# Performance work log

Hardware: AMD Instinct MI355X
Metric: run time of the kernel (lower is better)

The kernel has to match this reference:

```python
import jax, jax.numpy as jnp
import numpy as np

N = 100_000   # nodes
E = 600_000   # edges per layer (avg degree ~6, ogbn-arxiv-like)
IN, H, C = 128, 256, 40


def _sage_layer(x, src, dst, w_self, w_neigh, b):
    """DGL SAGEConv with mean aggregator: fc_self(x) + fc_neigh(mean_nbr) + b."""
    n = x.shape[0]
    msg = x[src]                                               # [E, d] gather
    agg = jax.ops.segment_sum(msg, dst, num_segments=n)        # [N, d]
    deg = jax.ops.segment_sum(jnp.ones((src.shape[0],), x.dtype), dst,
                              num_segments=n)                  # [N]
    h_neigh = agg / jnp.maximum(deg, 1.0)[:, None]             # mean; 0 if isolated
    return x @ w_self.T + h_neigh @ w_neigh.T + b


def setup_inputs() -> dict:
    key = jax.random.key(0)
    ks = jax.random.split(key, 11)
    s = 0.02
    return {
        "x": jax.random.normal(ks[0], (N, IN), jnp.float32),
        "src1": jax.random.randint(ks[1], (E,), 0, N, jnp.int32),
        "dst1": jax.random.randint(ks[2], (E,), 0, N, jnp.int32),
        "src2": jax.random.randint(ks[3], (E,), 0, N, jnp.int32),
        "dst2": jax.random.randint(ks[4], (E,), 0, N, jnp.int32),
        "w_self1": s * jax.random.normal(ks[5], (H, IN), jnp.float32),
        "w_neigh1": s * jax.random.normal(ks[6], (H, IN), jnp.float32),
        "b1": jnp.zeros((H,), jnp.float32),
        "w_self2": s * jax.random.normal(ks[7], (C, H), jnp.float32),
        "w_neigh2": s * jax.random.normal(ks[8], (C, H), jnp.float32),
        "b2": jnp.zeros((C,), jnp.float32),
    }


def reference(x, src1, dst1, src2, dst2, w_self1, w_neigh1, b1,
              w_self2, w_neigh2, b2):
    h = jax.nn.relu(_sage_layer(x, src1, dst1, w_self1, w_neigh1, b1))
    return _sage_layer(h, src2, dst2, w_self2, w_neigh2, b2)
```

## Files before the change

kernel.cpp:

```cpp
#include <hip/hip_runtime.h>
#include <hip/hip_bf16.h>
#include <cstdint>
#include <cstddef>


#define D_IN 128
#define D_H  256
#define D_C  40

#define NBLK     128
#define NBKT_MAX 392
#define BKT_CAP  2560

typedef __bf16 bf16_t;
typedef __attribute__((ext_vector_type(8))) __bf16 bf16x8;
typedef __attribute__((ext_vector_type(4))) float  f32x4;

static constexpr size_t NMAX = 100000;
static constexpr size_t EMAX = 600000;
static constexpr size_t NSC_MAX = (size_t)NBKT_MAX * NBLK;
static constexpr size_t alignup(size_t v) { return (v + 255) & ~size_t(255); }

static constexpr size_t HG1_OFF  = 0;
static constexpr size_t HG2_OFF  = alignup(HG1_OFF + NSC_MAX * 4);
static constexpr size_t BS1_OFF  = alignup(HG2_OFF + NSC_MAX * 4);
static constexpr size_t BS2_OFF  = alignup(BS1_OFF + 512 * 4);
static constexpr size_t RP1_OFF  = alignup(BS2_OFF + 512 * 4);
static constexpr size_t RP2_OFF  = alignup(RP1_OFF + (NMAX + 1) * 4);
static constexpr size_t BKT1_OFF = alignup(RP2_OFF + (NMAX + 1) * 4);
static constexpr size_t BKT2_OFF = alignup(BKT1_OFF + EMAX * 4);
static constexpr size_t XCAT_OFF = alignup(BKT2_OFF + EMAX * 4);
static constexpr size_t P_OFF    = alignup(XCAT_OFF + (NMAX + 64) * 256 * 2);
static constexpr size_t W1F_OFF  = alignup(P_OFF + NMAX * 40 * 4);
static constexpr size_t W2F_OFF  = alignup(W1F_OFF + 32 * 256 * 8 * 2);
static constexpr size_t WS_NEEDED = W2F_OFF + 32 * 80 * 8 * 2;

__global__ __launch_bounds__(256) void k_prep(
    const float* __restrict__ x, bf16_t* __restrict__ xcat,
    const float* __restrict__ ws1, const float* __restrict__ wn1,
    const float* __restrict__ ws2, const float* __restrict__ wn2,
    bf16_t* __restrict__ w1f, bf16_t* __restrict__ w2f,
    const int* __restrict__ dst1, const int* __restrict__ dst2,
    int* __restrict__ hg1, int* __restrict__ hg2,
    int N, int E, int chunk, int nbkt, int nconvx) {
  __shared__ int h[NBKT_MAX];
  int bid = blockIdx.x;

  if (bid < nconvx) {
    int t = bid * 256 + threadIdx.x;
    if (t < N * 16) {
      int row = t >> 4, j = t & 15;
      const float* sp = x + (size_t)row * 128 + j * 8;
      float4 v0 = ((const float4*)sp)[0];
      float4 v1 = ((const float4*)sp)[1];
      bf16x8 o;
      o[0] = (bf16_t)v0.x; o[1] = (bf16_t)v0.y; o[2] = (bf16_t)v0.z; o[3] = (bf16_t)v0.w;
      o[4] = (bf16_t)v1.x; o[5] = (bf16_t)v1.y; o[6] = (bf16_t)v1.z; o[7] = (bf16_t)v1.w;
      *(bf16x8*)(xcat + (size_t)row * 256 + j * 8) = o;
    }
    return;
  }
  bid -= nconvx;

  if (bid < 32) {
    int t = bid * 256 + threadIdx.x;
    {
      int ks4g = t >> 8, col = t & 255;
      int k0 = (ks4g >> 2) * 32 + (ks4g & 3) * 8;
      bf16x8 o;
#pragma unroll
      for (int i = 0; i < 8; ++i) {
        int k = k0 + i;
        float v = (k < 128) ? ws1[col * 128 + k] : wn1[col * 128 + (k - 128)];
        o[i] = (bf16_t)v;
      }
      *(bf16x8*)(w1f + (size_t)t * 8) = o;
    }
    if (t < 32 * 80) {
      int ks4g = t / 80, col = t - ks4g * 80;
      int k0 = (ks4g >> 2) * 32 + (ks4g & 3) * 8;
      bf16x8 o;
#pragma unroll
      for (int i = 0; i < 8; ++i) {
        int k = k0 + i;
        float v = (col < 40) ? ws2[col * 256 + k] : wn2[(col - 40) * 256 + k];
        o[i] = (bf16_t)v;
      }
      *(bf16x8*)(w2f + (size_t)t * 8) = o;
    }
    return;
  }
  bid -= 32;
  {
    const int* dst = (bid >> 7) ? dst2 : dst1;
    int*       hg  = (bid >> 7) ? hg2 : hg1;
    int        cb  = bid & 127;
    for (int i = threadIdx.x; i < nbkt; i += 256) h[i] = 0;
    __syncthreads();
    int beg = cb * chunk, end = min(E, beg + chunk);
    for (int e = beg + threadIdx.x; e < end; e += 256)
      atomicAdd(&h[dst[e] >> 8], 1);
    __syncthreads();
    for (int b = threadIdx.x; b < nbkt; b += 256)
      hg[b * NBLK + cb] = h[b];
  }
}

__global__ void k_scan_block(int* __restrict__ a1, int* __restrict__ a2,
                             int* __restrict__ b1s, int* __restrict__ b2s, int n) {
  int* a    = blockIdx.y ? a2 : a1;
  int* bsum = blockIdx.y ? b2s : b1s;
  __shared__ int lds[256];
  int t = threadIdx.x, i = blockIdx.x * 256 + t;
  int v = (i < n) ? a[i] : 0;
  lds[t] = v;
  __syncthreads();
  for (int off = 1; off < 256; off <<= 1) {
    int add = (t >= off) ? lds[t - off] : 0;
    __syncthreads();
    lds[t] += add;
    __syncthreads();
  }
  if (i < n) a[i] = lds[t] - v;
  if (t == 255) bsum[blockIdx.x] = lds[255];
}

__global__ void k_scan_sums(int* __restrict__ b1s, int* __restrict__ b2s, int nb) {
  int* bsum = blockIdx.x ? b2s : b1s;
  __shared__ int lds[512];
  int t = threadIdx.x;
  int v = (t < nb) ? bsum[t] : 0;
  lds[t] = v;
  __syncthreads();
  for (int off = 1; off < 512; off <<= 1) {
    int add = (t >= off) ? lds[t - off] : 0;
    __syncthreads();
    lds[t] += add;
    __syncthreads();
  }
  if (t < nb) bsum[t] = lds[t] - v;
}

__global__ void k_scan_add(int* __restrict__ a1, int* __restrict__ a2,
                           const int* __restrict__ b1s, const int* __restrict__ b2s, int n) {
  int* a        = blockIdx.y ? a2 : a1;
  const int* bs = blockIdx.y ? b2s : b1s;
  int i = blockIdx.x * 256 + threadIdx.x;
  if (i < n) a[i] += bs[i >> 8];
}

__global__ void k_scat(const int* __restrict__ src1, const int* __restrict__ dst1,
                       const int* __restrict__ src2, const int* __restrict__ dst2,
                       const int* __restrict__ off1, const int* __restrict__ off2,
                       unsigned* __restrict__ bkt1, unsigned* __restrict__ bkt2,
                       int E, int chunk, int nbkt) {
  const int* src = blockIdx.y ? src2 : src1;
  const int* dst = blockIdx.y ? dst2 : dst1;
  const int* off = blockIdx.y ? off2 : off1;
  unsigned*  bkt = blockIdx.y ? bkt2 : bkt1;
  __shared__ int cur[NBKT_MAX];
  for (int i = threadIdx.x; i < nbkt; i += 256)
    cur[i] = off[i * NBLK + blockIdx.x];
  __syncthreads();
  int beg = blockIdx.x * chunk, end = min(E, beg + chunk);
  for (int e = beg + threadIdx.x; e < end; e += 256) {
    int d = dst[e];
    int slot = atomicAdd(&cur[d >> 8], 1);
    bkt[slot] = (unsigned)src[e] | ((unsigned)(d & 255) << 24);
  }
}

__global__ __launch_bounds__(256) void k_bcsr(
    const int* __restrict__ off1, const int* __restrict__ off2,
    const unsigned* bkt1, const unsigned* bkt2,
    int* csr1, int* csr2,
    int* __restrict__ rp1, int* __restrict__ rp2, int E, int N, int nbkt) {
  const int* off      = blockIdx.y ? off2 : off1;
  const unsigned* bkt = blockIdx.y ? bkt2 : bkt1;
  int* csr            = blockIdx.y ? csr2 : csr1;
  int* rowptr         = blockIdx.y ? rp2 : rp1;

  const int b = blockIdx.x, t = threadIdx.x;
  const int base = off[b * NBLK];
  const int endp = (b == nbkt - 1) ? E : off[(b + 1) * NBLK];
  const int cnt  = endp - base;

  __shared__ int hist[256];
  __shared__ int sc[256];
  __shared__ int cur[256];
  __shared__ int stage[BKT_CAP];

  hist[t] = 0;
  __syncthreads();
  for (int i = t; i < cnt; i += 256)
    atomicAdd(&hist[bkt[base + i] >> 24], 1);
  __syncthreads();

  int v = hist[t];
  sc[t] = v;
  __syncthreads();
  for (int off_ = 1; off_ < 256; off_ <<= 1) {
    int add = (t >= off_) ? sc[t - off_] : 0;
    __syncthreads();
    sc[t] += add;
    __syncthreads();
  }
  int excl = sc[t] - v;

  int node = b * 256 + t;
  if (node < N) rowptr[node] = base + excl;
  if (b == nbkt - 1 && t == 0) rowptr[N] = E;
  cur[t] = excl;
  __syncthreads();

  for (int i = t; i < cnt; i += 256) {
    unsigned u = bkt[base + i];
    int slot = atomicAdd(&cur[u >> 24], 1);
    if (slot < BKT_CAP) stage[slot] = (int)(u & 0xFFFFFFu);
  }
  __syncthreads();
  for (int i = t; i < cnt; i += 256)
    csr[base + i] = stage[i];
}

__global__ void k_agg1(bf16_t* __restrict__ xcat, const int* __restrict__ rowptr,
                       const int* __restrict__ csr, int N) {
  int t = blockIdx.x * 256 + threadIdx.x;
  int node = t >> 4, l = t & 15;
  if (node >= N) return;
  int beg = rowptr[node], end = rowptr[node + 1];
  float acc[8] = {0.f, 0.f, 0.f, 0.f, 0.f, 0.f, 0.f, 0.f};
  for (int e = beg; e < end; ++e) {
    int s = csr[e];
    bf16x8 v = *(const bf16x8*)(xcat + (size_t)s * 256 + l * 8);
#pragma unroll
    for (int i = 0; i < 8; ++i) acc[i] += (float)v[i];
  }
  float rd = (end > beg) ? 1.0f / (float)(end - beg) : 0.0f;
  bf16x8 o;
#pragma unroll
  for (int i = 0; i < 8; ++i) o[i] = (bf16_t)(acc[i] * rd);
  *(bf16x8*)(xcat + (size_t)node * 256 + 128 + l * 8) = o;
}

__global__ __launch_bounds__(256, 4) void k_fused(
    const bf16_t* __restrict__ xcat, const bf16_t* __restrict__ w1f,
    const float* __restrict__ b1, const bf16_t* __restrict__ w2f,
    const float* __restrict__ b2v, float* __restrict__ out,
    float* __restrict__ p, int N) {
  __shared__ __align__(16) char lds[32768];
  const int m0   = blockIdx.x * 64;
  const int wv   = threadIdx.x >> 6;
  const int lane = threadIdx.x & 63;
  const int lr   = lane & 15;
  const int lg   = lane >> 4;
  const int c0   = wv * 64;

  {
    const char* tbase = (const char*)(xcat + (size_t)m0 * 256);
#pragma unroll
    for (int i = 0; i < 8; ++i) {
      int L   = i * 4096 + (int)threadIdx.x * 16;
      int row = L >> 9;
      int c   = L & 511;
      int so  = (row << 9) | (c ^ ((row & 7) << 4));
      __builtin_amdgcn_global_load_lds(
          (const __attribute__((address_space(1))) void*)(tbase + so),
          (__attribute__((address_space(3))) void*)(lds + L), 16, 0, 0);
    }
  }
  __syncthreads();

  f32x4 acc[4][4] = {};
#pragma unroll
  for (int ks = 0; ks < 8; ++ks) {
    bf16x8 a[4];
#pragma unroll
    for (int m = 0; m < 4; ++m) {
      int lrow = m * 16 + lr;
      int c    = ks * 64 + lg * 16;
      a[m] = *(const bf16x8*)(lds + lrow * 512 + (c ^ ((lrow & 7) << 4)));
    }
    bf16x8 b[4];
#pragma unroll
    for (int bn = 0; bn < 4; ++bn) {
      int col = c0 + bn * 16 + lr;
      b[bn] = *(const bf16x8*)(w1f + ((size_t)(ks * 4 + lg) * 256 + col) * 8);
    }
#pragma unroll
    for (int m = 0; m < 4; ++m)
#pragma unroll
      for (int bn = 0; bn < 4; ++bn)
        acc[m][bn] = __builtin_amdgcn_mfma_f32_16x16x32_bf16(a[m], b[bn], acc[m][bn], 0, 0, 0);
  }
  __syncthreads();

#pragma unroll
  for (int bn = 0; bn < 4; ++bn) {
    int   col  = c0 + bn * 16 + lr;
    float bias = b1[col];
#pragma unroll
    for (int m = 0; m < 4; ++m) {
#pragma unroll
      for (int i = 0; i < 4; ++i) {
        int row = m * 16 + lg * 4 + i;
        float v = acc[m][bn][i] + bias;
        *(bf16_t*)(lds + row * 512 + ((col * 2) ^ ((row & 7) << 4))) =
            (bf16_t)fmaxf(v, 0.0f);
      }
    }
  }
  __syncthreads();

  f32x4 acc2[5] = {};
  const int arow = wv * 16 + lr;
#pragma unroll
  for (int ks = 0; ks < 8; ++ks) {
    int c = ks * 64 + lg * 16;
    bf16x8 a2 = *(const bf16x8*)(lds + arow * 512 + (c ^ ((arow & 7) << 4)));
#pragma unroll
    for (int bn = 0; bn < 5; ++bn) {
      int col = bn * 16 + lr;
      bf16x8 bb = *(const bf16x8*)(w2f + ((size_t)(ks * 4 + lg) * 80 + col) * 8);
      acc2[bn] = __builtin_amdgcn_mfma_f32_16x16x32_bf16(a2, bb, acc2[bn], 0, 0, 0);
    }
  }

#pragma unroll
  for (int bn = 0; bn < 5; ++bn) {
    int col = bn * 16 + lr;
#pragma unroll
    for (int i = 0; i < 4; ++i) {
      int r = m0 + wv * 16 + lg * 4 + i;
      if (r < N) {
        float v = acc2[bn][i];
        if (col < 40) out[(size_t)r * 40 + col] = v + b2v[col];
        else          p[(size_t)r * 40 + (col - 40)] = v;
      }
    }
  }
}

__global__ void k_agg2fin(const float* __restrict__ p, const int* __restrict__ rowptr,
                          const int* __restrict__ csr, float* __restrict__ out, int N) {
  int t = blockIdx.x * 256 + threadIdx.x;
  int node = t / 10, l = t - node * 10;
  if (node >= N) return;
  int beg = rowptr[node], end = rowptr[node + 1];
  float4 acc = {0.f, 0.f, 0.f, 0.f};
  for (int e = beg; e < end; ++e) {
    int s = csr[e];
    float4 v = *(const float4*)(p + (size_t)s * 40 + l * 4);
    acc.x += v.x; acc.y += v.y; acc.z += v.z; acc.w += v.w;
  }
  float rd = (end > beg) ? 1.0f / (float)(end - beg) : 0.0f;
  float* o = out + (size_t)node * 40 + l * 4;
  float4 cur = *(const float4*)o;
  cur.x += acc.x * rd;
  cur.y += acc.y * rd;
  cur.z += acc.z * rd;
  cur.w += acc.w * rd;
  *(float4*)o = cur;
}

extern "C" void kernel_launch(void* const* d_in, const int* in_sizes, int n_in,
                              void* d_out, int out_size, void* d_ws, size_t ws_size,
                              hipStream_t stream) {
  const float* x    = (const float*)d_in[0];
  const int*   src1 = (const int*)d_in[1];
  const int*   dst1 = (const int*)d_in[2];
  const int*   src2 = (const int*)d_in[3];
  const int*   dst2 = (const int*)d_in[4];
  const float* ws1  = (const float*)d_in[5];
  const float* wn1  = (const float*)d_in[6];
  const float* b1   = (const float*)d_in[7];
  const float* ws2  = (const float*)d_in[8];
  const float* wn2  = (const float*)d_in[9];
  const float* b2   = (const float*)d_in[10];
  float*       out  = (float*)d_out;

  const int N = in_sizes[0] / D_IN;
  const int E = in_sizes[1];
  if (ws_size < WS_NEEDED) return;

  char*     ws   = (char*)d_ws;
  int*      hg1  = (int*)(ws + HG1_OFF);
  int*      hg2  = (int*)(ws + HG2_OFF);
  int*      bs1  = (int*)(ws + BS1_OFF);
  int*      bs2  = (int*)(ws + BS2_OFF);
  int*      rp1  = (int*)(ws + RP1_OFF);
  int*      rp2  = (int*)(ws + RP2_OFF);
  unsigned* bkt1 = (unsigned*)(ws + BKT1_OFF);
  unsigned* bkt2 = (unsigned*)(ws + BKT2_OFF);
  int*      csr1 = (int*)(ws + BKT1_OFF);
  int*      csr2 = (int*)(ws + BKT2_OFF);
  bf16_t*   xcat = (bf16_t*)(ws + XCAT_OFF);
  float*    p    = (float*)(ws + P_OFF);
  bf16_t*   w1f  = (bf16_t*)(ws + W1F_OFF);
  bf16_t*   w2f  = (bf16_t*)(ws + W2F_OFF);

  const int nbkt  = (N + 255) >> 8;
  const int chunk = (E + NBLK - 1) / NBLK;
  const int nsc   = nbkt * NBLK;
  const int nscb  = (nsc + 255) / 256;
  const int nconvx = (N * 16 + 255) / 256;

  k_prep<<<nconvx + 32 + 2 * NBLK, 256, 0, stream>>>(
      x, xcat, ws1, wn1, ws2, wn2, w1f, w2f, dst1, dst2, hg1, hg2,
      N, E, chunk, nbkt, nconvx);

  k_scan_block<<<dim3(nscb, 2), 256, 0, stream>>>(hg1, hg2, bs1, bs2, nsc);
  k_scan_sums<<<2, 512, 0, stream>>>(bs1, bs2, nscb);
  k_scan_add<<<dim3(nscb, 2), 256, 0, stream>>>(hg1, hg2, bs1, bs2, nsc);
  k_scat<<<dim3(NBLK, 2), 256, 0, stream>>>(src1, dst1, src2, dst2, hg1, hg2,
                                            bkt1, bkt2, E, chunk, nbkt);
  k_bcsr<<<dim3(nbkt, 2), 256, 0, stream>>>(hg1, hg2, bkt1, bkt2, csr1, csr2,
                                            rp1, rp2, E, N, nbkt);

  k_agg1<<<(N * 16 + 255) / 256, 256, 0, stream>>>(xcat, rp1, csr1, N);
  k_fused<<<(N + 63) / 64, 256, 0, stream>>>(xcat, w1f, b1, w2f, b2, out, p, N);
  k_agg2fin<<<(N * 10 + 255) / 256, 256, 0, stream>>>(p, rp2, csr2, out, N);
}
```

Before: 151.9 us.

## Make fused GEMM kernel persistent with double-buffered LDS tile prefetch

Turns the fused two-layer GEMM kernel into a persistent kernel with a grid capped at 512 blocks. Each block loops over 64-row tiles and prefetches the next tile into a second 32KB LDS buffer with async global-to-LDS loads while computing the current one. The goal is to hide the xcat load latency and avoid per-block launch and prologue cost. In exchange LDS doubles to 64KB and occupancy drops to 2 blocks per CU, and correctness now depends on hand-written waitcnt and barrier placement.

```diff
diff --git a/kernel.cpp b/kernel.cpp
--- a/kernel.cpp
+++ b/kernel.cpp
@@ -243,102 +243,126 @@
   *(bf16x8*)(xcat + (size_t)node * 256 + 128 + l * 8) = o;
 }
 
-__global__ __launch_bounds__(256, 4) void k_fused(
+__global__ __launch_bounds__(256, 2) void k_fused(
     const bf16_t* __restrict__ xcat, const bf16_t* __restrict__ w1f,
     const float* __restrict__ b1, const bf16_t* __restrict__ w2f,
     const float* __restrict__ b2v, float* __restrict__ out,
-    float* __restrict__ p, int N) {
-  __shared__ __align__(16) char lds[32768];
-  const int m0   = blockIdx.x * 64;
-  const int wv   = threadIdx.x >> 6;
-  const int lane = threadIdx.x & 63;
+    float* __restrict__ p, int N, int ntiles) {
+  __shared__ __align__(16) char lds[65536];
+  const int tid  = (int)threadIdx.x;
+  const int wv   = tid >> 6;
+  const int lane = tid & 63;
   const int lr   = lane & 15;
   const int lg   = lane >> 4;
   const int c0   = wv * 64;
 
-  {
-    const char* tbase = (const char*)(xcat + (size_t)m0 * 256);
-#pragma unroll
-    for (int i = 0; i < 8; ++i) {
-      int L   = i * 4096 + (int)threadIdx.x * 16;
-      int row = L >> 9;
-      int c   = L & 511;
-      int so  = (row << 9) | (c ^ ((row & 7) << 4));
-      __builtin_amdgcn_global_load_lds(
-          (const __attribute__((address_space(1))) void*)(tbase + so),
-          (__attribute__((address_space(3))) void*)(lds + L), 16, 0, 0);
-    }
-  }
-  __syncthreads();
-
-  f32x4 acc[4][4] = {};
-#pragma unroll
-  for (int ks = 0; ks < 8; ++ks) {
-    bf16x8 a[4];
-#pragma unroll
-    for (int m = 0; m < 4; ++m) {
-      int lrow = m * 16 + lr;
-      int c    = ks * 64 + lg * 16;
-      a[m] = *(const bf16x8*)(lds + lrow * 512 + (c ^ ((lrow & 7) << 4)));
-    }
-    bf16x8 b[4];
-#pragma unroll
-    for (int bn = 0; bn < 4; ++bn) {
-      int col = c0 + bn * 16 + lr;
-      b[bn] = *(const bf16x8*)(w1f + ((size_t)(ks * 4 + lg) * 256 + col) * 8);
-    }
-#pragma unroll
-    for (int m = 0; m < 4; ++m)
-#pragma unroll
-      for (int bn = 0; bn < 4; ++bn)
-        acc[m][bn] = __builtin_amdgcn_mfma_f32_16x16x32_bf16(a[m], b[bn], acc[m][bn], 0, 0, 0);
-  }
-  __syncthreads();
-
-#pragma unroll
-  for (int bn = 0; bn < 4; ++bn) {
-    int   col  = c0 + bn * 16 + lr;
-    float bias = b1[col];
-#pragma unroll
-    for (int m = 0; m < 4; ++m) {
+  char* bc = lds;
+  char* bn = lds + 32768;
+
+#define STAGE_TILE(DST, TILE)                                                  \
+  do {                                                                         \
+    const char* tb_ = (const char*)(xcat + (size_t)(TILE) * (64 * 256));       \
+    _Pragma("unroll")                                                          \
+    for (int i_ = 0; i_ < 8; ++i_) {                                           \
+      int L_   = i_ * 4096 + tid * 16;                                         \
+      int row_ = L_ >> 9;                                                      \
+      int c_   = L_ & 511;                                                     \
+      int so_  = (row_ << 9) | (c_ ^ ((row_ & 7) << 4));                       \
+      __builtin_amdgcn_global_load_lds(                                        \
+          (const __attribute__((address_space(1))) void*)(tb_ + so_),          \
+          (__attribute__((address_space(3))) void*)((DST) + L_), 16, 0, 0);    \
+    }                                                                          \
+  } while (0)
+
+  const int t0 = (int)blockIdx.x;
+  if (t0 < ntiles) STAGE_TILE(bc, t0);
+
+  for (int t = t0; t < ntiles; t += (int)gridDim.x) {
+    const int m0 = t * 64;
+    const int tn = t + (int)gridDim.x;
+    if (tn < ntiles) {
+      STAGE_TILE(bn, tn);
+      asm volatile("s_waitcnt vmcnt(8)" ::: "memory");
+    } else {
+      asm volatile("s_waitcnt vmcnt(0)" ::: "memory");
+    }
+    __builtin_amdgcn_s_barrier();
+
+    f32x4 acc[4][4] = {};
+#pragma unroll
+    for (int ks = 0; ks < 8; ++ks) {
+      bf16x8 a[4];
+#pragma unroll
+      for (int m = 0; m < 4; ++m) {
+        int lrow = m * 16 + lr;
+        int c    = ks * 64 + lg * 16;
+        a[m] = *(const bf16x8*)(bc + lrow * 512 + (c ^ ((lrow & 7) << 4)));
+      }
+      bf16x8 b[4];
+#pragma unroll
+      for (int bn_ = 0; bn_ < 4; ++bn_) {
+        int col = c0 + bn_ * 16 + lr;
+        b[bn_] = *(const bf16x8*)(w1f + ((size_t)(ks * 4 + lg) * 256 + col) * 8);
+      }
+#pragma unroll
+      for (int m = 0; m < 4; ++m)
+#pragma unroll
+        for (int bn_ = 0; bn_ < 4; ++bn_)
+          acc[m][bn_] = __builtin_amdgcn_mfma_f32_16x16x32_bf16(a[m], b[bn_], acc[m][bn_], 0, 0, 0);
+    }
+    asm volatile("s_waitcnt lgkmcnt(0)" ::: "memory");
+    __builtin_amdgcn_s_barrier();
+
+#pragma unroll
+    for (int bn_ = 0; bn_ < 4; ++bn_) {
+      int   col  = c0 + bn_ * 16 + lr;
+      float bias = b1[col];
+#pragma unroll
+      for (int m = 0; m < 4; ++m) {
+#pragma unroll
+        for (int i = 0; i < 4; ++i) {
+          int row = m * 16 + lg * 4 + i;
+          float v = acc[m][bn_][i] + bias;
+          *(bf16_t*)(bc + row * 512 + ((col * 2) ^ ((row & 7) << 4))) =
+              (bf16_t)fmaxf(v, 0.0f);
+        }
+      }
+    }
+    asm volatile("s_waitcnt lgkmcnt(0)" ::: "memory");
+    __builtin_amdgcn_s_barrier();
+
+    f32x4 acc2[5] = {};
+    const int arow = wv * 16 + lr;
+#pragma unroll
+    for (int ks = 0; ks < 8; ++ks) {
+      int c = ks * 64 + lg * 16;
+      bf16x8 a2 = *(const bf16x8*)(bc + arow * 512 + (c ^ ((arow & 7) << 4)));
+#pragma unroll
+      for (int bn_ = 0; bn_ < 5; ++bn_) {
+        int col = bn_ * 16 + lr;
+        bf16x8 bb = *(const bf16x8*)(w2f + ((size_t)(ks * 4 + lg) * 80 + col) * 8);
+        acc2[bn_] = __builtin_amdgcn_mfma_f32_16x16x32_bf16(a2, bb, acc2[bn_], 0, 0, 0);
+      }
+    }
+#pragma unroll
+    for (int bn_ = 0; bn_ < 5; ++bn_) {
+      int col = bn_ * 16 + lr;
 #pragma unroll
       for (int i = 0; i < 4; ++i) {
-        int row = m * 16 + lg * 4 + i;
-        float v = acc[m][bn][i] + bias;
-        *(bf16_t*)(lds + row * 512 + ((col * 2) ^ ((row & 7) << 4))) =
-            (bf16_t)fmaxf(v, 0.0f);
-      }
-    }
-  }
-  __syncthreads();
-
-  f32x4 acc2[5] = {};
-  const int arow = wv * 16 + lr;
-#pragma unroll
-  for (int ks = 0; ks < 8; ++ks) {
-    int c = ks * 64 + lg * 16;
-    bf16x8 a2 = *(const bf16x8*)(lds + arow * 512 + (c ^ ((arow & 7) << 4)));
-#pragma unroll
-    for (int bn = 0; bn < 5; ++bn) {
-      int col = bn * 16 + lr;
-      bf16x8 bb = *(const bf16x8*)(w2f + ((size_t)(ks * 4 + lg) * 80 + col) * 8);
-      acc2[bn] = __builtin_amdgcn_mfma_f32_16x16x32_bf16(a2, bb, acc2[bn], 0, 0, 0);
-    }
-  }
-
-#pragma unroll
-  for (int bn = 0; bn < 5; ++bn) {
-    int col = bn * 16 + lr;
-#pragma unroll
-    for (int i = 0; i < 4; ++i) {
-      int r = m0 + wv * 16 + lg * 4 + i;
-      if (r < N) {
-        float v = acc2[bn][i];
-        if (col < 40) out[(size_t)r * 40 + col] = v + b2v[col];
-        else          p[(size_t)r * 40 + (col - 40)] = v;
-      }
-    }
-  }
+        int r = m0 + wv * 16 + lg * 4 + i;
+        if (r < N) {
+          float v = acc2[bn_][i];
+          if (col < 40) out[(size_t)r * 40 + col] = v + b2v[col];
+          else          p[(size_t)r * 40 + (col - 40)] = v;
+        }
+      }
+    }
+    asm volatile("s_waitcnt lgkmcnt(0)" ::: "memory");
+    __builtin_amdgcn_s_barrier();
+
+    char* tmp = bc; bc = bn; bn = tmp;
+  }
+#undef STAGE_TILE
 }
 
 __global__ void k_agg2fin(const float* __restrict__ p, const int* __restrict__ rowptr,
@@ -404,6 +428,7 @@
   const int nsc   = nbkt * NBLK;
   const int nscb  = (nsc + 255) / 256;
   const int nconvx = (N * 16 + 255) / 256;
+  const int ntiles = (N + 63) / 64;
 
   k_prep<<<nconvx + 32 + 2 * NBLK, 256, 0, stream>>>(
       x, xcat, ws1, wn1, ws2, wn2, w1f, w2f, dst1, dst2, hg1, hg2,
@@ -418,6 +443,9 @@
                                             rp1, rp2, E, N, nbkt);
 
   k_agg1<<<(N * 16 + 255) / 256, 256, 0, stream>>>(xcat, rp1, csr1, N);
-  k_fused<<<(N + 63) / 64, 256, 0, stream>>>(xcat, w1f, b1, w2f, b2, out, p, N);
+  {
+    int grid = ntiles < 512 ? ntiles : 512;
+    k_fused<<<grid, 256, 0, stream>>>(xcat, w1f, b1, w2f, b2, out, p, N, ntiles);
+  }
   k_agg2fin<<<(N * 10 + 255) / 256, 256, 0, stream>>>(p, rp2, csr2, out, N);
 }
```

Measured after the change: 200.5 us. +31.9%, slower.

## Preload weights into registers and swap MFMA operands for vectorized epilogues

Applied to the files above, without the earlier changes.

The fused GEMM kernel now loads all of its layer-1 weight fragments into registers before the barrier, so they overlap with the async LDS tile load. It also preloads the layer-2 weights ahead of the second GEMM. The MFMA operands are swapped (weights as A, activations as B), so each lane holds four consecutive output columns. That lets the bias+ReLU writeback to LDS and the final out/p stores become vector stores instead of scalar ones. Removing the occupancy hint from launch bounds and holding 72 bf16x8 register arrays raises register pressure and may lower occupancy or cause spills.

```diff
diff --git a/kernel.cpp b/kernel.cpp
--- a/kernel.cpp
+++ b/kernel.cpp
@@ -14,6 +14,7 @@
 
 typedef __bf16 bf16_t;
 typedef __attribute__((ext_vector_type(8))) __bf16 bf16x8;
+typedef __attribute__((ext_vector_type(4))) __bf16 bf16x4;
 typedef __attribute__((ext_vector_type(4))) float  f32x4;
 
 static constexpr size_t NMAX = 100000;
@@ -243,71 +244,85 @@
   *(bf16x8*)(xcat + (size_t)node * 256 + 128 + l * 8) = o;
 }
 
-__global__ __launch_bounds__(256, 4) void k_fused(
+__global__ __launch_bounds__(256) void k_fused(
     const bf16_t* __restrict__ xcat, const bf16_t* __restrict__ w1f,
     const float* __restrict__ b1, const bf16_t* __restrict__ w2f,
     const float* __restrict__ b2v, float* __restrict__ out,
     float* __restrict__ p, int N) {
   __shared__ __align__(16) char lds[32768];
-  const int m0   = blockIdx.x * 64;
-  const int wv   = threadIdx.x >> 6;
-  const int lane = threadIdx.x & 63;
+  const int tid  = (int)threadIdx.x;
+  const int wv   = tid >> 6;
+  const int lane = tid & 63;
   const int lr   = lane & 15;
   const int lg   = lane >> 4;
   const int c0   = wv * 64;
+  const int m0   = (int)blockIdx.x * 64;
 
   {
-    const char* tbase = (const char*)(xcat + (size_t)m0 * 256);
+    const char* tb = (const char*)(xcat + (size_t)m0 * 256);
 #pragma unroll
     for (int i = 0; i < 8; ++i) {
-      int L   = i * 4096 + (int)threadIdx.x * 16;
+      int L   = i * 4096 + tid * 16;
       int row = L >> 9;
       int c   = L & 511;
       int so  = (row << 9) | (c ^ ((row & 7) << 4));
       __builtin_amdgcn_global_load_lds(
-          (const __attribute__((address_space(1))) void*)(tbase + so),
+          (const __attribute__((address_space(1))) void*)(tb + so),
           (__attribute__((address_space(3))) void*)(lds + L), 16, 0, 0);
     }
   }
+
+  bf16x8 wf[8][4];
+#pragma unroll
+  for (int ks = 0; ks < 8; ++ks)
+#pragma unroll
+    for (int wb = 0; wb < 4; ++wb)
+      wf[ks][wb] = *(const bf16x8*)(w1f + ((size_t)(ks * 4 + lg) * 256 +
+                                           (c0 + wb * 16 + lr)) * 8);
+
   __syncthreads();
 
   f32x4 acc[4][4] = {};
 #pragma unroll
   for (int ks = 0; ks < 8; ++ks) {
-    bf16x8 a[4];
-#pragma unroll
-    for (int m = 0; m < 4; ++m) {
-      int lrow = m * 16 + lr;
-      int c    = ks * 64 + lg * 16;
-      a[m] = *(const bf16x8*)(lds + lrow * 512 + (c ^ ((lrow & 7) << 4)));
-    }
-    bf16x8 b[4];
-#pragma unroll
-    for (int bn = 0; bn < 4; ++bn) {
-      int col = c0 + bn * 16 + lr;
-      b[bn] = *(const bf16x8*)(w1f + ((size_t)(ks * 4 + lg) * 256 + col) * 8);
-    }
-#pragma unroll
-    for (int m = 0; m < 4; ++m)
-#pragma unroll
-      for (int bn = 0; bn < 4; ++bn)
-        acc[m][bn] = __builtin_amdgcn_mfma_f32_16x16x32_bf16(a[m], b[bn], acc[m][bn], 0, 0, 0);
-  }
-  __syncthreads();
-
-#pragma unroll
-  for (int bn = 0; bn < 4; ++bn) {
-    int   col  = c0 + bn * 16 + lr;
-    float bias = b1[col];
-#pragma unroll
-    for (int m = 0; m < 4; ++m) {
-#pragma unroll
-      for (int i = 0; i < 4; ++i) {
-        int row = m * 16 + lg * 4 + i;
-        float v = acc[m][bn][i] + bias;
-        *(bf16_t*)(lds + row * 512 + ((col * 2) ^ ((row & 7) << 4))) =
-            (bf16_t)fmaxf(v, 0.0f);
-      }
+    bf16x8 ax[4];
+#pragma unroll
+    for (int rb = 0; rb < 4; ++rb) {
+      int lrow = rb * 16 + lr;
+      ax[rb] = *(const bf16x8*)(lds + lrow * 512 +
+                                ((ks * 64 + lg * 16) ^ ((lrow & 7) << 4)));
+    }
+#pragma unroll
+    for (int wb = 0; wb < 4; ++wb)
+#pragma unroll
+      for (int rb = 0; rb < 4; ++rb)
+        acc[wb][rb] = __builtin_amdgcn_mfma_f32_16x16x32_bf16(
+            wf[ks][wb], ax[rb], acc[wb][rb], 0, 0, 0);
+  }
+
+  bf16x8 w2r[8][5];
+#pragma unroll
+  for (int ks = 0; ks < 8; ++ks)
+#pragma unroll
+    for (int wb = 0; wb < 5; ++wb)
+      w2r[ks][wb] = *(const bf16x8*)(w2f + ((size_t)(ks * 4 + lg) * 80 +
+                                            (wb * 16 + lr)) * 8);
+
+  __syncthreads();
+
+#pragma unroll
+  for (int wb = 0; wb < 4; ++wb) {
+    float4 b4 = *(const float4*)(b1 + c0 + wb * 16 + lg * 4);
+#pragma unroll
+    for (int rb = 0; rb < 4; ++rb) {
+      int xrow = rb * 16 + lr;
+      bf16x4 o;
+      o[0] = (bf16_t)fmaxf(acc[wb][rb][0] + b4.x, 0.f);
+      o[1] = (bf16_t)fmaxf(acc[wb][rb][1] + b4.y, 0.f);
+      o[2] = (bf16_t)fmaxf(acc[wb][rb][2] + b4.z, 0.f);
+      o[3] = (bf16_t)fmaxf(acc[wb][rb][3] + b4.w, 0.f);
+      *(bf16x4*)(lds + xrow * 512 +
+                 ((c0 * 2 + wb * 32 + lg * 8) ^ ((xrow & 7) << 4))) = o;
     }
   }
   __syncthreads();
@@ -316,26 +331,26 @@
   const int arow = wv * 16 + lr;
 #pragma unroll
   for (int ks = 0; ks < 8; ++ks) {
-    int c = ks * 64 + lg * 16;
-    bf16x8 a2 = *(const bf16x8*)(lds + arow * 512 + (c ^ ((arow & 7) << 4)));
-#pragma unroll
-    for (int bn = 0; bn < 5; ++bn) {
-      int col = bn * 16 + lr;
-      bf16x8 bb = *(const bf16x8*)(w2f + ((size_t)(ks * 4 + lg) * 80 + col) * 8);
-      acc2[bn] = __builtin_amdgcn_mfma_f32_16x16x32_bf16(a2, bb, acc2[bn], 0, 0, 0);
-    }
-  }
-
-#pragma unroll
-  for (int bn = 0; bn < 5; ++bn) {
-    int col = bn * 16 + lr;
-#pragma unroll
-    for (int i = 0; i < 4; ++i) {
-      int r = m0 + wv * 16 + lg * 4 + i;
-      if (r < N) {
-        float v = acc2[bn][i];
-        if (col < 40) out[(size_t)r * 40 + col] = v + b2v[col];
-        else          p[(size_t)r * 40 + (col - 40)] = v;
+    bf16x8 hf = *(const bf16x8*)(lds + arow * 512 +
+                                 ((ks * 64 + lg * 16) ^ ((arow & 7) << 4)));
+#pragma unroll
+    for (int wb = 0; wb < 5; ++wb)
+      acc2[wb] = __builtin_amdgcn_mfma_f32_16x16x32_bf16(
+          w2r[ks][wb], hf, acc2[wb], 0, 0, 0);
+  }
+
+  const int r = m0 + wv * 16 + lr;
+  if (r < N) {
+#pragma unroll
+    for (int wb = 0; wb < 5; ++wb) {
+      int col0 = wb * 16 + lg * 4;
+      f32x4 v = acc2[wb];
+      if (col0 < 40) {
+        float4 b4 = *(const float4*)(b2v + col0);
+        v[0] += b4.x; v[1] += b4.y; v[2] += b4.z; v[3] += b4.w;
+        *(f32x4*)(out + (size_t)r * 40 + col0) = v;
+      } else {
+        *(f32x4*)(p + (size_t)r * 40 + (col0 - 40)) = v;
       }
     }
   }
@@ -404,6 +419,7 @@
   const int nsc   = nbkt * NBLK;
   const int nscb  = (nsc + 255) / 256;
   const int nconvx = (N * 16 + 255) / 256;
+  const int ntiles = (N + 63) / 64;
 
   k_prep<<<nconvx + 32 + 2 * NBLK, 256, 0, stream>>>(
       x, xcat, ws1, wn1, ws2, wn2, w1f, w2f, dst1, dst2, hg1, hg2,
@@ -418,6 +434,6 @@
                                             rp1, rp2, E, N, nbkt);
 
   k_agg1<<<(N * 16 + 255) / 256, 256, 0, stream>>>(xcat, rp1, csr1, N);
-  k_fused<<<(N + 63) / 64, 256, 0, stream>>>(xcat, w1f, b1, w2f, b2, out, p, N);
+  k_fused<<<ntiles, 256, 0, stream>>>(xcat, w1f, b1, w2f, b2, out, p, N);
   k_agg2fin<<<(N * 10 + 255) / 256, 256, 0, stream>>>(p, rp2, csr2, out, N);
 }
```

Measured after the change: 155.7 us. 2.5% more time.
